# Performance work log

Measured on AMD Instinct MI355X. Metric: run time of the kernel, lower is better.

The kernel has to match this reference:

```python
import jax, jax.numpy as jnp
import numpy as np

B, Lq, C, NH, NP, DFF = 8, 10000, 256, 8, 4, 1024
H_IMG, W_IMG = 100, 100
HD = C // NH


def _layer_norm(x, g, b, eps=1e-5):
    m = jnp.mean(x, -1, keepdims=True)
    v = jnp.mean((x - m) ** 2, -1, keepdims=True)
    return (x - m) / jnp.sqrt(v + eps) * g + b


def _bilinear_sample(value, loc, Hs, Ws):
    # value: [B, Lin, NH, HD]; loc: [B, Lq, NH, NP, 2] normalized to [0,1]
    vt = jnp.transpose(value, (0, 2, 1, 3))  # [B, NH, Lin, HD]
    # move to [B, NH, Lq, NP] layout once; grid_sample(align_corners=False) pixel coords
    x = jnp.transpose(loc[..., 0], (0, 2, 1, 3)) * Ws - 0.5
    y = jnp.transpose(loc[..., 1], (0, 2, 1, 3)) * Hs - 0.5
    x0 = jnp.floor(x); y0 = jnp.floor(y)
    lx = x - x0; ly = y - y0

    def corner(xi, yi, w):
        valid = (xi >= 0) & (xi < Ws) & (yi >= 0) & (yi < Hs)
        xc = jnp.clip(xi, 0, Ws - 1).astype(jnp.int32)
        yc = jnp.clip(yi, 0, Hs - 1).astype(jnp.int32)
        idx = (yc * Ws + xc).reshape(B, NH, Lq * NP, 1)
        v = jnp.take_along_axis(vt, idx, axis=2).reshape(B, NH, Lq, NP, HD)
        return v * (w * valid)[..., None]

    acc = corner(x0, y0, (1 - lx) * (1 - ly))
    acc = acc + corner(x0 + 1, y0, lx * (1 - ly))
    acc = acc + corner(x0, y0 + 1, (1 - lx) * ly)
    acc = acc + corner(x0 + 1, y0 + 1, lx * ly)
    return acc  # [B, NH, Lq, NP, HD]


def setup_inputs() -> dict:
    key = jax.random.key(0)
    ks = jax.random.split(key, 12)
    s = 0.02
    return {
        "query": jax.random.normal(ks[0], (B, Lq, C), jnp.float32),
        "src": jax.random.normal(ks[1], (B, H_IMG * W_IMG, C), jnp.float32),
        "reference_points": jax.random.uniform(ks[2], (B, Lq, 1, 2), jnp.float32),
        "spatial_shapes": jnp.array([[H_IMG, W_IMG]], dtype=jnp.int64),
        "level_start_index": jnp.array([0], dtype=jnp.int64),
        "W_off": jax.random.normal(ks[3], (C, NH * NP * 2), jnp.float32) * s,
        "b_off": jnp.zeros((NH * NP * 2,), jnp.float32),
        "W_aw": jax.random.normal(ks[4], (C, NH * NP), jnp.float32) * s,
        "b_aw": jnp.zeros((NH * NP,), jnp.float32),
        "W_val": jax.random.normal(ks[5], (C, C), jnp.float32) * s,
        "b_val": jnp.zeros((C,), jnp.float32),
        "W_out": jax.random.normal(ks[6], (C, C), jnp.float32) * s,
        "b_out": jnp.zeros((C,), jnp.float32),
        "g1": jnp.ones((C,), jnp.float32),
        "be1": jnp.zeros((C,), jnp.float32),
        "W1": jax.random.normal(ks[7], (C, DFF), jnp.float32) * s,
        "b1": jnp.zeros((DFF,), jnp.float32),
        "W2": jax.random.normal(ks[8], (DFF, C), jnp.float32) * s,
        "b2": jnp.zeros((C,), jnp.float32),
        "g2": jnp.ones((C,), jnp.float32),
        "be2": jnp.zeros((C,), jnp.float32),
    }


def reference(query, src, reference_points, spatial_shapes, level_start_index,
              W_off, b_off, W_aw, b_aw, W_val, b_val, W_out, b_out,
              g1, be1, W1, b1, W2, b2, g2, be2):
    Hs = spatial_shapes[0, 0]
    Ws = spatial_shapes[0, 1]
    # MSDeformAttn (n_levels = 1)
    value = (src @ W_val + b_val).reshape(B, -1, NH, HD)
    off = (query @ W_off + b_off).reshape(B, Lq, NH, NP, 2)
    aw = jax.nn.softmax((query @ W_aw + b_aw).reshape(B, Lq, NH, NP), axis=-1)
    normalizer = jnp.stack([Ws, Hs]).astype(query.dtype)  # (W, H)
    loc = reference_points[:, :, None] + off / normalizer  # [B,Lq,NH,NP,2]
    sampled = _bilinear_sample(value, loc, Hs, Ws)  # [B,NH,Lq,NP,HD]
    attn = jnp.einsum('bhqpd,bqhp->bqhd', sampled, aw).reshape(B, Lq, C)
    attn = attn @ W_out + b_out
    # residual + LN + FFN + LN
    q = _layer_norm(query + attn, g1, be1)
    ffn = jax.nn.relu(q @ W1 + b1) @ W2 + b2
    return _layer_norm(q + ffn, g2, be2)
```

## Files before the change

kernel.cpp:

```cpp
#include <hip/hip_runtime.h>
#include <hip/hip_bf16.h>

typedef __hip_bfloat16 bf16;
typedef unsigned short u16;
typedef short short8 __attribute__((ext_vector_type(8)));
typedef float f32x4 __attribute__((ext_vector_type(4)));

static constexpr int B_   = 8;
static constexpr int Lq_  = 10000;
static constexpr int C_   = 256;
static constexpr int NH_  = 8;
static constexpr int NP_  = 4;
static constexpr int HIMG = 100;
static constexpr int WIMG = 100;
static constexpr int LIN  = 10000;

__device__ __forceinline__ u16 f2bf(float x) {
    union { bf16 b; u16 u; } cv; cv.b = __float2bfloat16(x); return cv.u;
}
__device__ __forceinline__ float bf2f(u16 u) {
    return __uint_as_float((unsigned)u << 16);
}

__device__ __forceinline__ void gl_lds16(const void* g, void* l) {
    __builtin_amdgcn_global_load_lds(
        (const __attribute__((address_space(1))) void*)g,
        (__attribute__((address_space(3))) void*)l, 16, 0, 0);
}
__device__ __forceinline__ void drain_barrier() {
    asm volatile("s_waitcnt vmcnt(0) lgkmcnt(0)" ::: "memory");
    __builtin_amdgcn_s_barrier();
}
#define LKW0() asm volatile("s_waitcnt lgkmcnt(0)" ::: "memory")
#define BAR()  __builtin_amdgcn_s_barrier()

template <bool AF32, bool LN>
__global__ __launch_bounds__(512, 2) void gemm256(
    const void* __restrict__ Av, const u16* __restrict__ Bg,
    const float* __restrict__ bias, const float* __restrict__ resid,
    const float* __restrict__ gw, const float* __restrict__ bw,
    u16* __restrict__ Co, int K)
{
    __shared__ __align__(16) u16 At[2][128 * 64];
    __shared__ __align__(16) u16 Bt[2][256 * 64];
    __shared__ float red[2][128][4];

    const int tid  = threadIdx.x;
    const int lane = tid & 63;
    const int w    = tid >> 6;
    const int wm   = w >> 2, wn = w & 3;
    const int m0   = blockIdx.x * 128;

    f32x4 acc[4][4];
#pragma unroll
    for (int i = 0; i < 4; ++i)
#pragma unroll
        for (int j = 0; j < 4; ++j) acc[i][j] = f32x4{0.f, 0.f, 0.f, 0.f};

    auto stageA = [&](int t) {
        const int kt = t << 6;
        if constexpr (AF32) {
            const int row = tid >> 2;
            const int k0  = (tid & 3) << 4;
            const float* s = (const float*)Av + (size_t)(m0 + row) * K + kt + k0;
            float4 v0 = *(const float4*)(s + 0);
            float4 v1 = *(const float4*)(s + 4);
            float4 v2 = *(const float4*)(s + 8);
            float4 v3 = *(const float4*)(s + 12);
            union { short8 s8; u16 u[8]; } ga, gb;
            ga.u[0]=f2bf(v0.x); ga.u[1]=f2bf(v0.y); ga.u[2]=f2bf(v0.z); ga.u[3]=f2bf(v0.w);
            ga.u[4]=f2bf(v1.x); ga.u[5]=f2bf(v1.y); ga.u[6]=f2bf(v1.z); ga.u[7]=f2bf(v1.w);
            gb.u[0]=f2bf(v2.x); gb.u[1]=f2bf(v2.y); gb.u[2]=f2bf(v2.z); gb.u[3]=f2bf(v2.w);
            gb.u[4]=f2bf(v3.x); gb.u[5]=f2bf(v3.y); gb.u[6]=f2bf(v3.z); gb.u[7]=f2bf(v3.w);
            u16* d = &At[t & 1][row * 64];
            *(short8*)&d[(k0)     ^ ((row & 7) << 3)] = ga.s8;
            *(short8*)&d[(k0 + 8) ^ ((row & 7) << 3)] = gb.s8;
        } else {
#pragma unroll
            for (int i = 0; i < 2; ++i) {
                const int rb  = w * 16 + i * 8;
                const int row = rb + (lane >> 3);
                const int gs  = (lane & 7) ^ (row & 7);
                gl_lds16((const u16*)Av + (size_t)(m0 + row) * K + kt + gs * 8,
                         &At[t & 1][rb * 64]);
            }
        }
    };
    auto stageB = [&](int t) {
        const int kt = t << 6;
#pragma unroll
        for (int i = 0; i < 4; ++i) {
            const int rb  = w * 32 + i * 8;
            const int row = rb + (lane >> 3);
            gl_lds16(Bg + (size_t)row * K + kt + (lane & 7) * 8,
                     &Bt[t & 1][rb * 64]);
        }
    };
    auto compute = [&](int t) {
        const u16* a = At[t & 1];
        const u16* b = Bt[t & 1];
#pragma unroll
        for (int ks = 0; ks < 2; ++ks) {
            const int ko = ks * 32 + ((lane >> 4) << 3);
            short8 bfr[4];
#pragma unroll
            for (int n = 0; n < 4; ++n) {
                const int nr = wn * 64 + n * 16 + (lane & 15);
                bfr[n] = *(const short8*)&b[nr * 64 + (ko ^ ((nr & 7) << 3))];
            }
#pragma unroll
            for (int m = 0; m < 4; ++m) {
                const int ar = wm * 64 + m * 16 + (lane & 15);
                const short8 af = *(const short8*)&a[ar * 64 + (ko ^ ((ar & 7) << 3))];
#pragma unroll
                for (int n = 0; n < 4; ++n)
                    acc[m][n] = __builtin_amdgcn_mfma_f32_16x16x32_bf16(
                        af, bfr[n], acc[m][n], 0, 0, 0);
            }
        }
    };

    stageA(0); stageB(0);
    drain_barrier();
    const int nt = K >> 6;
    for (int t = 0; t < nt; ++t) {
        if (t + 1 < nt) { stageA(t + 1); stageB(t + 1); }
        compute(t);
        drain_barrier();
    }

    float bcol[4], gcol[4], becol[4];
#pragma unroll
    for (int n = 0; n < 4; ++n) {
        const int col = wn * 64 + n * 16 + (lane & 15);
        bcol[n] = bias[col];
        if (LN) { gcol[n] = gw[col]; becol[n] = bw[col]; }
    }

    if constexpr (!LN) {
#pragma unroll
        for (int m = 0; m < 4; ++m)
#pragma unroll
            for (int r = 0; r < 4; ++r) {
                const int lr = wm * 64 + m * 16 + (lane >> 4) * 4 + r;
#pragma unroll
                for (int n = 0; n < 4; ++n) {
                    const int col = wn * 64 + n * 16 + (lane & 15);
                    Co[(size_t)(m0 + lr) * 256 + col] = f2bf(acc[m][n][r] + bcol[n]);
                }
            }
    } else {
        float s[4][4], s2[4][4];
#pragma unroll
        for (int m = 0; m < 4; ++m)
#pragma unroll
            for (int r = 0; r < 4; ++r) {
                const int lr = wm * 64 + m * 16 + (lane >> 4) * 4 + r;
                float ps = 0.f, ps2 = 0.f;
#pragma unroll
                for (int n = 0; n < 4; ++n) {
                    const int col = wn * 64 + n * 16 + (lane & 15);
                    float v = acc[m][n][r] + bcol[n]
                            + resid[(size_t)(m0 + lr) * 256 + col];
                    acc[m][n][r] = v;
                    ps += v; ps2 += v * v;
                }
#pragma unroll
                for (int o = 1; o < 16; o <<= 1) {
                    ps  += __shfl_xor(ps,  o);
                    ps2 += __shfl_xor(ps2, o);
                }
                s[m][r] = ps; s2[m][r] = ps2;
            }
        if ((lane & 15) == 0) {
#pragma unroll
            for (int m = 0; m < 4; ++m)
#pragma unroll
                for (int r = 0; r < 4; ++r) {
                    const int lr = wm * 64 + m * 16 + (lane >> 4) * 4 + r;
                    red[0][lr][wn] = s[m][r];
                    red[1][lr][wn] = s2[m][r];
                }
        }
        __syncthreads();
        if (tid < 128) {
            const float ss  = red[0][tid][0] + red[0][tid][1] + red[0][tid][2] + red[0][tid][3];
            const float ss2 = red[1][tid][0] + red[1][tid][1] + red[1][tid][2] + red[1][tid][3];
            const float mean = ss * (1.f / 256.f);
            const float var  = fmaxf(ss2 * (1.f / 256.f) - mean * mean, 0.f);
            red[0][tid][0] = mean;
            red[1][tid][0] = rsqrtf(var + 1e-5f);
        }
        __syncthreads();
#pragma unroll
        for (int m = 0; m < 4; ++m)
#pragma unroll
            for (int r = 0; r < 4; ++r) {
                const int lr = wm * 64 + m * 16 + (lane >> 4) * 4 + r;
                const float mean = red[0][lr][0];
                const float rstd = red[1][lr][0];
#pragma unroll
                for (int n = 0; n < 4; ++n) {
                    const int col = wn * 64 + n * 16 + (lane & 15);
                    const float o = (acc[m][n][r] - mean) * rstd * gcol[n] + becol[n];
                    Co[(size_t)(m0 + lr) * 256 + (col ^ ((lr & 7) << 3))] = f2bf(o);
                }
            }
    }
}

__global__ __launch_bounds__(512) void ffn_fused(
    const u16* __restrict__ q1b, const u16* __restrict__ W1f,
    const u16* __restrict__ W2f, const float* __restrict__ b1,
    const float* __restrict__ b2, const float* __restrict__ g2w,
    const float* __restrict__ be2, float* __restrict__ out)
{
    __shared__ __align__(16) u16 Asl[2][128 * 64];
    __shared__ __align__(16) u16 Hs[128 * 136];
    __shared__ __align__(16) u16 B1s[2][128 * 64];
    __shared__ __align__(16) u16 B2s[2][256 * 32];
    float (*red)[128][4] = (float (*)[128][4])Hs;

    const int tid  = threadIdx.x;
    const int lane = tid & 63;
    const int w    = tid >> 6;
    const int wm   = w >> 2, wn = w & 3;
    const int m0   = blockIdx.x * 128;
    const int ko   = (lane >> 4) << 3;

    int arow[4], aswz[4], hrow[4];
#pragma unroll
    for (int m = 0; m < 4; ++m) {
        const int ar = wm * 64 + m * 16 + (lane & 15);
        arow[m] = ar * 64; aswz[m] = (ar & 7) << 3; hrow[m] = ar * 136;
    }
    int b1r[2], b1x[2];
#pragma unroll
    for (int q = 0; q < 2; ++q) {
        const int nr = wn * 32 + q * 16 + (lane & 15);
        b1r[q] = nr * 64; b1x[q] = (nr & 7) << 3;
    }
    int b2i[4];
#pragma unroll
    for (int q = 0; q < 4; ++q) {
        const int nr = wn * 64 + q * 16 + (lane & 15);
        const int pr = nr >> 1;
        b2i[q] = pr * 64 + (nr & 1) * 32 + (ko ^ ((pr & 3) << 3));
    }

    f32x4 acc2[4][4];
#pragma unroll
    for (int i = 0; i < 4; ++i)
#pragma unroll
        for (int j = 0; j < 4; ++j) acc2[i][j] = f32x4{0.f, 0.f, 0.f, 0.f};

    auto stageAs = [&](int t, int buf) {
#pragma unroll
        for (int i = 0; i < 2; ++i) {
            const int rb = w * 16 + i * 8;
            gl_lds16(q1b + (size_t)(m0 + rb + (lane >> 3)) * 256 + t * 64 + (lane & 7) * 8,
                     &Asl[buf][rb * 64]);
        }
    };
    auto stageB1 = [&](int c, int t, int buf) {
#pragma unroll
        for (int i = 0; i < 2; ++i)
            gl_lds16(W1f + (size_t)(c * 4 + t) * 8192 + w * 1024 + i * 512 + lane * 8,
                     &B1s[buf][w * 1024 + i * 512]);
    };
    auto stageB2 = [&](int c, int u, int buf) {
#pragma unroll
        for (int i = 0; i < 2; ++i)
            gl_lds16(W2f + (size_t)(c * 4 + u) * 8192 + w * 1024 + i * 512 + lane * 8,
                     &B2s[buf][w * 1024 + i * 512]);
    };

    stageAs(0, 0); stageB1(0, 0, 0);
    drain_barrier();

    for (int c = 0; c < 8; ++c) {
        f32x4 acc1[4][2];
#pragma unroll
        for (int i = 0; i < 4; ++i)
#pragma unroll
            for (int j = 0; j < 2; ++j) acc1[i][j] = f32x4{0.f, 0.f, 0.f, 0.f};

        auto g1 = [&](int t) {
            const u16* a = Asl[t & 1];
            const u16* b = B1s[t & 1];
            __builtin_amdgcn_s_setprio(1);
#pragma unroll
            for (int ks = 0; ks < 2; ++ks) {
                const int kk = ks * 32 + ko;
                short8 bfr[2];
#pragma unroll
                for (int q = 0; q < 2; ++q)
                    bfr[q] = *(const short8*)&b[b1r[q] + (kk ^ b1x[q])];
#pragma unroll
                for (int m = 0; m < 4; ++m) {
                    const short8 af = *(const short8*)&a[arow[m] + (kk ^ aswz[m])];
#pragma unroll
                    for (int q = 0; q < 2; ++q)
                        acc1[m][q] = __builtin_amdgcn_mfma_f32_16x16x32_bf16(
                            af, bfr[q], acc1[m][q], 0, 0, 0);
                }
            }
            __builtin_amdgcn_s_setprio(0);
        };
        auto g2 = [&](int u) {
            const u16* b = B2s[u & 1];
            __builtin_amdgcn_s_setprio(1);
            short8 bfr[4];
#pragma unroll
            for (int q = 0; q < 4; ++q)
                bfr[q] = *(const short8*)&b[b2i[q]];
#pragma unroll
            for (int m = 0; m < 4; ++m) {
                const short8 af = *(const short8*)&Hs[hrow[m] + u * 32 + ko];
#pragma unroll
                for (int q = 0; q < 4; ++q)
                    acc2[m][q] = __builtin_amdgcn_mfma_f32_16x16x32_bf16(
                        af, bfr[q], acc2[m][q], 0, 0, 0);
            }
            __builtin_amdgcn_s_setprio(0);
        };

        stageAs(1, 1); stageB1(c, 1, 1);                   g1(0); drain_barrier();
        stageAs(2, 0); stageB1(c, 2, 0);                   g1(1); drain_barrier();
        stageAs(3, 1); stageB1(c, 3, 1); stageB2(c, 0, 0); g1(2); drain_barrier();
        stageB2(c, 1, 1);                                  g1(3); drain_barrier();

#pragma unroll
        for (int q = 0; q < 2; ++q) {
            const int col = wn * 32 + q * 16 + (lane & 15);
            const float bv = b1[c * 128 + col];
#pragma unroll
            for (int m = 0; m < 4; ++m)
#pragma unroll
                for (int r = 0; r < 4; ++r) {
                    const int row = wm * 64 + m * 16 + (lane >> 4) * 4 + r;
                    Hs[row * 136 + col] = f2bf(fmaxf(acc1[m][q][r] + bv, 0.f));
                }
        }
        LKW0(); BAR();

        g2(0); drain_barrier();
        stageB2(c, 2, 0);                                  g2(1); drain_barrier();
        if (c < 7) { stageAs(0, 0); stageB1(c + 1, 0, 0); }
        stageB2(c, 3, 1);                                  g2(2); drain_barrier();
        g2(3); drain_barrier();
    }

    float bcol[4], gcol[4], becol[4];
#pragma unroll
    for (int n = 0; n < 4; ++n) {
        const int col = wn * 64 + n * 16 + (lane & 15);
        bcol[n] = b2[col]; gcol[n] = g2w[col]; becol[n] = be2[col];
    }
    float s[4][4], s2[4][4];
#pragma unroll
    for (int m = 0; m < 4; ++m)
#pragma unroll
        for (int r = 0; r < 4; ++r) {
            const int lr = wm * 64 + m * 16 + (lane >> 4) * 4 + r;
            float ps = 0.f, ps2 = 0.f;
#pragma unroll
            for (int n = 0; n < 4; ++n) {
                const int col = wn * 64 + n * 16 + (lane & 15);
                const float q = bf2f(q1b[(size_t)(m0 + lr) * 256 + (col ^ ((lr & 7) << 3))]);
                const float v = acc2[m][n][r] + bcol[n] + q;
                acc2[m][n][r] = v;
                ps += v; ps2 += v * v;
            }
#pragma unroll
            for (int o = 1; o < 16; o <<= 1) {
                ps  += __shfl_xor(ps,  o);
                ps2 += __shfl_xor(ps2, o);
            }
            s[m][r] = ps; s2[m][r] = ps2;
        }
    if ((lane & 15) == 0) {
#pragma unroll
        for (int m = 0; m < 4; ++m)
#pragma unroll
            for (int r = 0; r < 4; ++r) {
                const int lr = wm * 64 + m * 16 + (lane >> 4) * 4 + r;
                red[0][lr][wn] = s[m][r];
                red[1][lr][wn] = s2[m][r];
            }
    }
    __syncthreads();
    if (tid < 128) {
        const float ss  = red[0][tid][0] + red[0][tid][1] + red[0][tid][2] + red[0][tid][3];
        const float ss2 = red[1][tid][0] + red[1][tid][1] + red[1][tid][2] + red[1][tid][3];
        const float mean = ss * (1.f / 256.f);
        const float var  = fmaxf(ss2 * (1.f / 256.f) - mean * mean, 0.f);
        red[0][tid][0] = mean;
        red[1][tid][0] = rsqrtf(var + 1e-5f);
    }
    __syncthreads();
#pragma unroll
    for (int m = 0; m < 4; ++m)
#pragma unroll
        for (int r = 0; r < 4; ++r) {
            const int lr = wm * 64 + m * 16 + (lane >> 4) * 4 + r;
            const float mean = red[0][lr][0];
            const float rstd = red[1][lr][0];
#pragma unroll
            for (int n = 0; n < 4; ++n) {
                const int col = wn * 64 + n * 16 + (lane & 15);
                out[(size_t)(m0 + lr) * 256 + col] =
                    (acc2[m][n][r] - mean) * rstd * gcol[n] + becol[n];
            }
        }
}

__global__ __launch_bounds__(256) void gemm_oaw(
    const float* __restrict__ Av, const u16* __restrict__ Bt,
    const float* __restrict__ bias, float* __restrict__ C,
    int M, int K, int Nreal, int ldc)
{
    __shared__ __align__(16) u16 Asl[2][128 * 32];
    __shared__ __align__(16) u16 Bsl[2][128 * 32];

    const int tid  = threadIdx.x;
    const int lane = tid & 63;
    const int w    = tid >> 6;
    const int wr   = (w >> 1) * 64;
    const int wc   = (w & 1) * 64;
    const int m0   = blockIdx.y * 128;
    const int n0   = blockIdx.x * 128;

    const int srow = lane >> 2;
    const int scol = (lane & 3) << 3;
    const u16* bG = Bt + (size_t)(n0 + w * 32 + srow) * K + scol;
    const size_t rstep16 = (size_t)16 * K;

    const int ar  = lane >> 3;
    const int ac  = (lane & 7) << 2;
    const float* aGf = Av + (size_t)(m0 + w * 32 + ar) * K + ac;

    const int aRoff = (wr + (lane & 15)) * 32 + (lane >> 4) * 8;
    const int bRoff = (wc + (lane & 15)) * 32 + (lane >> 4) * 8;

    f32x4 acc[4][4];
#pragma unroll
    for (int i = 0; i < 4; ++i)
#pragma unroll
        for (int j = 0; j < 4; ++j) acc[i][j] = f32x4{0.f, 0.f, 0.f, 0.f};

    float4 a4[4];
    const int nt = K >> 5;

#pragma unroll
    for (int rep = 0; rep < 4; ++rep)
        a4[rep] = *(const float4*)(aGf + (size_t)(rep * 8) * K);
#pragma unroll
    for (int rep = 0; rep < 4; ++rep) {
        ushort4 v{f2bf(a4[rep].x), f2bf(a4[rep].y), f2bf(a4[rep].z), f2bf(a4[rep].w)};
        *(ushort4*)&Asl[0][(w * 32 + rep * 8 + ar) * 32 + ac] = v;
    }
    gl_lds16(bG, &Bsl[0][(w * 32) * 32]);
    gl_lds16(bG + rstep16, &Bsl[0][(w * 32 + 16) * 32]);
    drain_barrier();

    for (int t = 0; t < nt; ++t) {
        const int cur = t & 1, nxt = cur ^ 1;
        const int k0n = (t + 1) << 5;
        const bool has_next = (t + 1 < nt);
        if (has_next) {
#pragma unroll
            for (int rep = 0; rep < 4; ++rep)
                a4[rep] = *(const float4*)(aGf + k0n + (size_t)(rep * 8) * K);
            gl_lds16(bG + k0n, &Bsl[nxt][(w * 32) * 32]);
            gl_lds16(bG + k0n + rstep16, &Bsl[nxt][(w * 32 + 16) * 32]);
        }
        short8 af[4], bfr[4];
#pragma unroll
        for (int m = 0; m < 4; ++m) af[m]  = *(const short8*)&Asl[cur][aRoff + m * 16 * 32];
#pragma unroll
        for (int n = 0; n < 4; ++n) bfr[n] = *(const short8*)&Bsl[cur][bRoff + n * 16 * 32];
#pragma unroll
        for (int m = 0; m < 4; ++m)
#pragma unroll
            for (int n = 0; n < 4; ++n)
                acc[m][n] = __builtin_amdgcn_mfma_f32_16x16x32_bf16(
                    af[m], bfr[n], acc[m][n], 0, 0, 0);
        if (has_next) {
#pragma unroll
            for (int rep = 0; rep < 4; ++rep) {
                ushort4 v{f2bf(a4[rep].x), f2bf(a4[rep].y), f2bf(a4[rep].z), f2bf(a4[rep].w)};
                *(ushort4*)&Asl[nxt][(w * 32 + rep * 8 + ar) * 32 + ac] = v;
            }
        }
        drain_barrier();
    }

#pragma unroll
    for (int n = 0; n < 4; ++n) {
        const int gc = n0 + wc + n * 16 + (lane & 15);
        if (gc >= Nreal) continue;
        const float bv = bias[gc];
        const int gr0 = m0 + wr + (lane >> 4) * 4;
#pragma unroll
        for (int m = 0; m < 4; ++m)
#pragma unroll
            for (int r = 0; r < 4; ++r)
                C[(size_t)(gr0 + m * 16 + r) * ldc + gc] = acc[m][n][r] + bv;
    }
}

__global__ __launch_bounds__(256) void prep_all(
    const float* __restrict__ Wv, const float* __restrict__ Wo,
    const float* __restrict__ W1, const float* __restrict__ W2,
    const float* __restrict__ Woff, const float* __restrict__ Waw,
    const float* __restrict__ boff, const float* __restrict__ baw,
    u16* __restrict__ Wvs, u16* __restrict__ Wos,
    u16* __restrict__ W1f, u16* __restrict__ W2f,
    u16* __restrict__ Woa, float* __restrict__ boa)
{
    const int idx = blockIdx.x * 256 + threadIdx.x;
    if (idx < 65536) {
        const int n = idx >> 8, kd = idx & 255;
        Wvs[idx] = f2bf(Wv[(size_t)(kd ^ ((n & 7) << 3)) * 256 + n]);
    } else if (idx < 131072) {
        const int i = idx - 65536, n = i >> 8, kd = i & 255;
        Wos[i] = f2bf(Wo[(size_t)(kd ^ ((n & 7) << 3)) * 256 + n]);
    } else if (idx < 393216) {
        const int i = idx - 131072;
        const int tile = i >> 13, si = i & 8191;
        const int c = tile >> 2, t = tile & 3;
        const int n = si >> 6, kd = si & 63;
        W1f[i] = f2bf(W1[(size_t)(t * 64 + (kd ^ ((n & 7) << 3))) * 1024 + c * 128 + n]);
    } else if (idx < 655360) {
        const int i = idx - 393216;
        const int tile = i >> 13, si = i & 8191;
        const int c = tile >> 2, u = tile & 3;
        const int pr = si >> 6, h = (si >> 5) & 1, e = si & 31;
        const int n = (pr << 1) | h;
        W2f[i] = f2bf(W2[(size_t)(c * 128 + u * 32 + (e ^ ((pr & 3) << 3))) * 256 + n]);
    } else if (idx < 688128) {
        const int i = idx - 655360, n = i >> 8, k = i & 255;
        float v = 0.f;
        if (n < 64)      v = Woff[(size_t)k * 64 + n];
        else if (n < 96) v = Waw[(size_t)k * 32 + (n - 64)];
        Woa[i] = f2bf(v);
    } else if (idx < 688256) {
        const int i = idx - 688128;
        boa[i] = (i < 64) ? boff[i] : (i < 96 ? baw[i - 64] : 0.f);
    }
}

__global__ __launch_bounds__(256) void sample_attn(
    const u16* __restrict__ val, const float* __restrict__ oaw,
    const float* __restrict__ refp, u16* __restrict__ attn)
{
    const int t   = threadIdx.x;
    const int gid = blockIdx.x * 64 + (t >> 2);
    const int c0  = (t & 3) << 3;
    const int h   = gid & (NH_ - 1);
    const int bq  = gid >> 3;

    const float* row = oaw + (size_t)bq * 96;
    const float rx = refp[(size_t)bq * 2 + 0] * (float)WIMG;
    const float ry = refp[(size_t)bq * 2 + 1] * (float)HIMG;

    const float4 aw4 = *(const float4*)(row + 64 + h * 4);
    const float mx = fmaxf(fmaxf(aw4.x, aw4.y), fmaxf(aw4.z, aw4.w));
    const float e0 = __expf(aw4.x - mx), e1 = __expf(aw4.y - mx);
    const float e2 = __expf(aw4.z - mx), e3 = __expf(aw4.w - mx);
    const float inv = 1.f / (e0 + e1 + e2 + e3);
    const float w4[4] = {e0 * inv, e1 * inv, e2 * inv, e3 * inv};

    const int b = bq / Lq_;
    const u16* vb = val + (size_t)b * LIN * C_ + h * 32 + c0;

    float acc[8] = {};
#pragma unroll
    for (int p = 0; p < NP_; ++p) {
        const float2 off = *(const float2*)(row + (h * 4 + p) * 2);
        const float x = rx + off.x - 0.5f;
        const float y = ry + off.y - 0.5f;
        const float xf = floorf(x), yf = floorf(y);
        const float lx = x - xf, ly = y - yf;
        const int x0 = (int)xf, y0 = (int)yf;
        const float wp = w4[p];
        const float w00 = wp * (1.f - lx) * (1.f - ly);
        const float w10 = wp * lx * (1.f - ly);
        const float w01 = wp * (1.f - lx) * ly;
        const float w11 = wp * lx * ly;

#pragma unroll
        for (int c = 0; c < 4; ++c) {
            const int xi = x0 + (c & 1);
            const int yi = y0 + (c >> 1);
            const float wc = (c == 0) ? w00 : (c == 1) ? w10 : (c == 2) ? w01 : w11;
            const bool v = ((unsigned)xi < (unsigned)WIMG) & ((unsigned)yi < (unsigned)HIMG);
            const int idx = v ? (yi * WIMG + xi) : 0;
            const float w = v ? wc : 0.f;
            const short8 d = *(const short8*)(vb + (size_t)idx * C_);
#pragma unroll
            for (int j = 0; j < 8; ++j)
                acc[j] = fmaf(w, bf2f(((const u16*)&d)[j]), acc[j]);
        }
    }

    union { short8 s; u16 u[8]; } o;
#pragma unroll
    for (int j = 0; j < 8; ++j) o.u[j] = f2bf(acc[j]);
    *(short8*)(attn + (size_t)bq * C_ + h * 32 + c0) = o.s;
}

extern "C" void kernel_launch(void* const* d_in, const int* in_sizes, int n_in,
                              void* d_out, int out_size, void* d_ws, size_t ws_size,
                              hipStream_t stream)
{
    const float* query = (const float*)d_in[0];
    const float* src   = (const float*)d_in[1];
    const float* refp  = (const float*)d_in[2];
    const float* W_off = (const float*)d_in[5];
    const float* b_off = (const float*)d_in[6];
    const float* W_aw  = (const float*)d_in[7];
    const float* b_aw  = (const float*)d_in[8];
    const float* W_val = (const float*)d_in[9];
    const float* b_val = (const float*)d_in[10];
    const float* W_out = (const float*)d_in[11];
    const float* b_out = (const float*)d_in[12];
    const float* g1    = (const float*)d_in[13];
    const float* be1   = (const float*)d_in[14];
    const float* W1    = (const float*)d_in[15];
    const float* b1    = (const float*)d_in[16];
    const float* W2    = (const float*)d_in[17];
    const float* b2    = (const float*)d_in[18];
    const float* g2    = (const float*)d_in[19];
    const float* be2   = (const float*)d_in[20];
    float* out = (float*)d_out;

    char* ws = (char*)d_ws;
    const int R = B_ * Lq_;

    u16*  val  = (u16*)(ws + 0);
    float* oaw = (float*)(ws + 40960000);
    u16*  attn = (u16*)(ws + 71680000);
    u16*  q1b  = (u16*)(ws + 112640000);
    u16*  Wvs  = (u16*)(ws + 153600000);
    u16*  Wos  = (u16*)(ws + 153600000 + 131072);
    u16*  W1f  = (u16*)(ws + 153600000 + 262144);
    u16*  W2f  = (u16*)(ws + 153600000 + 786432);
    u16*  Woa  = (u16*)(ws + 153600000 + 1310720);
    float* boa = (float*)(ws + 153600000 + 1376256);

    prep_all<<<2689, 256, 0, stream>>>(W_val, W_out, W1, W2, W_off, W_aw,
                                       b_off, b_aw, Wvs, Wos, W1f, W2f,
                                       Woa, boa);

    gemm256<true, false><<<625, 512, 0, stream>>>(
        src, Wvs, b_val, nullptr, nullptr, nullptr, val, 256);

    gemm_oaw<<<dim3(1, 625), 256, 0, stream>>>(
        query, Woa, boa, oaw, R, 256, 96, 96);

    sample_attn<<<10000, 256, 0, stream>>>(val, oaw, refp, attn);

    gemm256<false, true><<<625, 512, 0, stream>>>(
        attn, Wos, b_out, query, g1, be1, q1b, 256);

    ffn_fused<<<625, 512, 0, stream>>>(q1b, W1f, W2f, b1, b2, g2, be2, out);
}
```

Baseline: 333.7 us.

## Replace FFN double-buffering with a 12-slot LDS ring and pre-tiled operand layout

The fused FFN kernel now streams A, W1 and W2 tiles through a 12-entry LDS ring with partial vmcnt waits, so loads run several stages ahead instead of draining all memory traffic at every barrier. The LN epilogue of the out-projection GEMM writes q1 directly in a pre-tiled, swizzled 4096-element tile layout, and W1/W2 are repacked to match, so each ring slot is one contiguous 8 KB copy. The b1 bias is staged in LDS. This adds complex ring indexing and more LDS use, which may limit occupancy.

```diff
diff --git a/kernel.cpp b/kernel.cpp
--- a/kernel.cpp
+++ b/kernel.cpp
@@ -31,8 +31,10 @@
     asm volatile("s_waitcnt vmcnt(0) lgkmcnt(0)" ::: "memory");
     __builtin_amdgcn_s_barrier();
 }
+#define VMW(N) asm volatile("s_waitcnt vmcnt(" #N ")" ::: "memory")
 #define LKW0() asm volatile("s_waitcnt lgkmcnt(0)" ::: "memory")
 #define BAR()  __builtin_amdgcn_s_barrier()
+
 
 template <bool AF32, bool LN>
 __global__ __launch_bounds__(512, 2) void gemm256(
@@ -203,22 +205,23 @@
                 for (int n = 0; n < 4; ++n) {
                     const int col = wn * 64 + n * 16 + (lane & 15);
                     const float o = (acc[m][n][r] - mean) * rstd * gcol[n] + becol[n];
-                    Co[(size_t)(m0 + lr) * 256 + (col ^ ((lr & 7) << 3))] = f2bf(o);
+                    const int tt = col >> 5, ccol = col & 31, pr = lr >> 1;
+                    Co[((size_t)blockIdx.x * 8 + tt) * 4096
+                       + pr * 64 + (lr & 1) * 32 + (ccol ^ ((pr & 3) << 3))] = f2bf(o);
                 }
             }
     }
 }
 
-__global__ __launch_bounds__(512) void ffn_fused(
-    const u16* __restrict__ q1b, const u16* __restrict__ W1f,
-    const u16* __restrict__ W2f, const float* __restrict__ b1,
+__global__ __launch_bounds__(512) void ffn_deep(
+    const u16* __restrict__ q1p, const u16* __restrict__ W1p,
+    const u16* __restrict__ W2p, const float* __restrict__ b1,
     const float* __restrict__ b2, const float* __restrict__ g2w,
     const float* __restrict__ be2, float* __restrict__ out)
 {
-    __shared__ __align__(16) u16 Asl[2][128 * 64];
-    __shared__ __align__(16) u16 Hs[128 * 136];
-    __shared__ __align__(16) u16 B1s[2][128 * 64];
-    __shared__ __align__(16) u16 B2s[2][256 * 32];
+    __shared__ __align__(16) u16 ring[12][4096];
+    __shared__ __align__(16) u16 Hs[4][4096];
+    __shared__ __align__(16) float b1L[1024];
     float (*red)[128][4] = (float (*)[128][4])Hs;
 
     const int tid  = threadIdx.x;
@@ -228,24 +231,26 @@
     const int m0   = blockIdx.x * 128;
     const int ko   = (lane >> 4) << 3;
 
-    int arow[4], aswz[4], hrow[4];
+    int aoff[4];
 #pragma unroll
     for (int m = 0; m < 4; ++m) {
         const int ar = wm * 64 + m * 16 + (lane & 15);
-        arow[m] = ar * 64; aswz[m] = (ar & 7) << 3; hrow[m] = ar * 136;
-    }
-    int b1r[2], b1x[2];
+        const int pa = ar >> 1;
+        aoff[m] = pa * 64 + (ar & 1) * 32 + (ko ^ ((pa & 3) << 3));
+    }
+    int b1off[2];
 #pragma unroll
     for (int q = 0; q < 2; ++q) {
         const int nr = wn * 32 + q * 16 + (lane & 15);
-        b1r[q] = nr * 64; b1x[q] = (nr & 7) << 3;
-    }
-    int b2i[4];
-#pragma unroll
-    for (int q = 0; q < 4; ++q) {
-        const int nr = wn * 64 + q * 16 + (lane & 15);
         const int pr = nr >> 1;
-        b2i[q] = pr * 64 + (nr & 1) * 32 + (ko ^ ((pr & 3) << 3));
+        b1off[q] = pr * 64 + (nr & 1) * 32 + (ko ^ ((pr & 3) << 3));
+    }
+    int b2off[4];
+#pragma unroll
+    for (int nf = 0; nf < 4; ++nf) {
+        const int nr = (wn & 1) * 64 + nf * 16 + (lane & 15);
+        const int pr = nr >> 1;
+        b2off[nf] = pr * 64 + (nr & 1) * 32 + (ko ^ ((pr & 3) << 3));
     }
 
     f32x4 acc2[4][4];
@@ -254,102 +259,95 @@
 #pragma unroll
         for (int j = 0; j < 4; ++j) acc2[i][j] = f32x4{0.f, 0.f, 0.f, 0.f};
 
-    auto stageAs = [&](int t, int buf) {
-#pragma unroll
-        for (int i = 0; i < 2; ++i) {
-            const int rb = w * 16 + i * 8;
-            gl_lds16(q1b + (size_t)(m0 + rb + (lane >> 3)) * 256 + t * 64 + (lane & 7) * 8,
-                     &Asl[buf][rb * 64]);
-        }
+    auto issue = [&](int g) {
+        if (g >= 192) g -= 192;
+        const int cc = g / 24;
+        const int r  = g - cc * 24;
+        const u16* src;
+        if (r < 16) {
+            const int t = r >> 1;
+            src = (r & 1) ? W1p + ((size_t)(cc * 8 + t)) * 4096
+                          : q1p + ((size_t)(blockIdx.x * 8 + t)) * 4096;
+        } else {
+            src = W2p + ((size_t)(cc * 8 + (r - 16))) * 4096;
+        }
+        gl_lds16(src + w * 512 + lane * 8, &ring[g % 12][w * 512]);
     };
-    auto stageB1 = [&](int c, int t, int buf) {
-#pragma unroll
-        for (int i = 0; i < 2; ++i)
-            gl_lds16(W1f + (size_t)(c * 4 + t) * 8192 + w * 1024 + i * 512 + lane * 8,
-                     &B1s[buf][w * 1024 + i * 512]);
-    };
-    auto stageB2 = [&](int c, int u, int buf) {
-#pragma unroll
-        for (int i = 0; i < 2; ++i)
-            gl_lds16(W2f + (size_t)(c * 4 + u) * 8192 + w * 1024 + i * 512 + lane * 8,
-                     &B2s[buf][w * 1024 + i * 512]);
-    };
-
-    stageAs(0, 0); stageB1(0, 0, 0);
-    drain_barrier();
-
-    for (int c = 0; c < 8; ++c) {
+
+    gl_lds16(b1 + (w & 3) * 256 + lane * 4, &b1L[(w & 3) * 256]);
+    for (int g = 0; g < 10; ++g) issue(g);
+    VMW(8); BAR();
+
+    int gbase = 0;
+    for (int c = 0; c < 8; ++c, gbase += 24) {
         f32x4 acc1[4][2];
 #pragma unroll
         for (int i = 0; i < 4; ++i)
 #pragma unroll
             for (int j = 0; j < 2; ++j) acc1[i][j] = f32x4{0.f, 0.f, 0.f, 0.f};
 
-        auto g1 = [&](int t) {
-            const u16* a = Asl[t & 1];
-            const u16* b = B1s[t & 1];
+#pragma unroll
+        for (int t = 0; t < 8; ++t) {
+            issue(gbase + 2 * t + 10);
+            issue(gbase + 2 * t + 11);
+            const u16* aT = ring[(2 * t) % 12];
+            const u16* bT = ring[(2 * t + 1) % 12];
+            const short8 bf0 = *(const short8*)&bT[b1off[0]];
+            const short8 bf1 = *(const short8*)&bT[b1off[1]];
             __builtin_amdgcn_s_setprio(1);
 #pragma unroll
-            for (int ks = 0; ks < 2; ++ks) {
-                const int kk = ks * 32 + ko;
-                short8 bfr[2];
-#pragma unroll
-                for (int q = 0; q < 2; ++q)
-                    bfr[q] = *(const short8*)&b[b1r[q] + (kk ^ b1x[q])];
-#pragma unroll
-                for (int m = 0; m < 4; ++m) {
-                    const short8 af = *(const short8*)&a[arow[m] + (kk ^ aswz[m])];
-#pragma unroll
-                    for (int q = 0; q < 2; ++q)
-                        acc1[m][q] = __builtin_amdgcn_mfma_f32_16x16x32_bf16(
-                            af, bfr[q], acc1[m][q], 0, 0, 0);
-                }
+            for (int m = 0; m < 4; ++m) {
+                const short8 af = *(const short8*)&aT[aoff[m]];
+                acc1[m][0] = __builtin_amdgcn_mfma_f32_16x16x32_bf16(
+                    af, bf0, acc1[m][0], 0, 0, 0);
+                acc1[m][1] = __builtin_amdgcn_mfma_f32_16x16x32_bf16(
+                    af, bf1, acc1[m][1], 0, 0, 0);
             }
             __builtin_amdgcn_s_setprio(0);
-        };
-        auto g2 = [&](int u) {
-            const u16* b = B2s[u & 1];
-            __builtin_amdgcn_s_setprio(1);
-            short8 bfr[4];
-#pragma unroll
-            for (int q = 0; q < 4; ++q)
-                bfr[q] = *(const short8*)&b[b2i[q]];
-#pragma unroll
-            for (int m = 0; m < 4; ++m) {
-                const short8 af = *(const short8*)&Hs[hrow[m] + u * 32 + ko];
-#pragma unroll
-                for (int q = 0; q < 4; ++q)
-                    acc2[m][q] = __builtin_amdgcn_mfma_f32_16x16x32_bf16(
-                        af, bfr[q], acc2[m][q], 0, 0, 0);
-            }
-            __builtin_amdgcn_s_setprio(0);
-        };
-
-        stageAs(1, 1); stageB1(c, 1, 1);                   g1(0); drain_barrier();
-        stageAs(2, 0); stageB1(c, 2, 0);                   g1(1); drain_barrier();
-        stageAs(3, 1); stageB1(c, 3, 1); stageB2(c, 0, 0); g1(2); drain_barrier();
-        stageB2(c, 1, 1);                                  g1(3); drain_barrier();
+            VMW(8); BAR();
+        }
 
 #pragma unroll
         for (int q = 0; q < 2; ++q) {
             const int col = wn * 32 + q * 16 + (lane & 15);
-            const float bv = b1[c * 128 + col];
+            const float bv = b1L[c * 128 + col];
+            const int ut = col >> 5, ccol = col & 31;
 #pragma unroll
             for (int m = 0; m < 4; ++m)
 #pragma unroll
                 for (int r = 0; r < 4; ++r) {
                     const int row = wm * 64 + m * 16 + (lane >> 4) * 4 + r;
-                    Hs[row * 136 + col] = f2bf(fmaxf(acc1[m][q][r] + bv, 0.f));
+                    const int pr = row >> 1;
+                    Hs[ut][pr * 64 + (row & 1) * 32 + (ccol ^ ((pr & 3) << 3))] =
+                        f2bf(fmaxf(acc1[m][q][r] + bv, 0.f));
                 }
         }
         LKW0(); BAR();
 
-        g2(0); drain_barrier();
-        stageB2(c, 2, 0);                                  g2(1); drain_barrier();
-        if (c < 7) { stageAs(0, 0); stageB1(c + 1, 0, 0); }
-        stageB2(c, 3, 1);                                  g2(2); drain_barrier();
-        g2(3); drain_barrier();
-    }
+#pragma unroll
+        for (int u = 0; u < 4; ++u) {
+            issue(gbase + 26 + 2 * u);
+            issue(gbase + 27 + 2 * u);
+            const u16* bT = ring[(16 + 2 * u + (wn >> 1)) % 12];
+            short8 bfr[4];
+#pragma unroll
+            for (int nf = 0; nf < 4; ++nf)
+                bfr[nf] = *(const short8*)&bT[b2off[nf]];
+            __builtin_amdgcn_s_setprio(1);
+#pragma unroll
+            for (int m = 0; m < 4; ++m) {
+                const short8 af = *(const short8*)&Hs[u][aoff[m]];
+#pragma unroll
+                for (int nf = 0; nf < 4; ++nf)
+                    acc2[m][nf] = __builtin_amdgcn_mfma_f32_16x16x32_bf16(
+                        af, bfr[nf], acc2[m][nf], 0, 0, 0);
+            }
+            __builtin_amdgcn_s_setprio(0);
+            VMW(8); BAR();
+        }
+    }
+    asm volatile("s_waitcnt vmcnt(0)" ::: "memory");
+    BAR();
 
     float bcol[4], gcol[4], becol[4];
 #pragma unroll
@@ -363,11 +361,14 @@
 #pragma unroll
         for (int r = 0; r < 4; ++r) {
             const int lr = wm * 64 + m * 16 + (lane >> 4) * 4 + r;
+            const int pr = lr >> 1;
             float ps = 0.f, ps2 = 0.f;
 #pragma unroll
             for (int n = 0; n < 4; ++n) {
                 const int col = wn * 64 + n * 16 + (lane & 15);
-                const float q = bf2f(q1b[(size_t)(m0 + lr) * 256 + (col ^ ((lr & 7) << 3))]);
+                const int tt = col >> 5, ccol = col & 31;
+                const float q = bf2f(q1p[((size_t)blockIdx.x * 8 + tt) * 4096
+                    + pr * 64 + (lr & 1) * 32 + (ccol ^ ((pr & 3) << 3))]);
                 const float v = acc2[m][n][r] + bcol[n] + q;
                 acc2[m][n][r] = v;
                 ps += v; ps2 += v * v;
@@ -516,7 +517,7 @@
     const float* __restrict__ Woff, const float* __restrict__ Waw,
     const float* __restrict__ boff, const float* __restrict__ baw,
     u16* __restrict__ Wvs, u16* __restrict__ Wos,
-    u16* __restrict__ W1f, u16* __restrict__ W2f,
+    u16* __restrict__ W1p, u16* __restrict__ W2p,
     u16* __restrict__ Woa, float* __restrict__ boa)
 {
     const int idx = blockIdx.x * 256 + threadIdx.x;
@@ -528,17 +529,21 @@
         Wos[i] = f2bf(Wo[(size_t)(kd ^ ((n & 7) << 3)) * 256 + n]);
     } else if (idx < 393216) {
         const int i = idx - 131072;
-        const int tile = i >> 13, si = i & 8191;
-        const int c = tile >> 2, t = tile & 3;
-        const int n = si >> 6, kd = si & 63;
-        W1f[i] = f2bf(W1[(size_t)(t * 64 + (kd ^ ((n & 7) << 3))) * 1024 + c * 128 + n]);
+        const int tile = i >> 12, si = i & 4095;
+        const int c = tile >> 3, t = tile & 7;
+        const int pr = si >> 6, h = (si >> 5) & 1, e = si & 31;
+        const int nr = (pr << 1) | h;
+        const int kk = e ^ ((pr & 3) << 3);
+        W1p[i] = f2bf(W1[(size_t)(t * 32 + kk) * 1024 + c * 128 + nr]);
     } else if (idx < 655360) {
         const int i = idx - 393216;
-        const int tile = i >> 13, si = i & 8191;
-        const int c = tile >> 2, u = tile & 3;
+        const int tile = i >> 12, si = i & 4095;
+        const int c = tile >> 3, j = tile & 7;
+        const int u = j >> 1, half = j & 1;
         const int pr = si >> 6, h = (si >> 5) & 1, e = si & 31;
-        const int n = (pr << 1) | h;
-        W2f[i] = f2bf(W2[(size_t)(c * 128 + u * 32 + (e ^ ((pr & 3) << 3))) * 256 + n]);
+        const int nr = (pr << 1) | h;
+        const int kk = e ^ ((pr & 3) << 3);
+        W2p[i] = f2bf(W2[(size_t)(c * 128 + u * 32 + kk) * 256 + half * 128 + nr]);
     } else if (idx < 688128) {
         const int i = idx - 655360, n = i >> 8, k = i & 255;
         float v = 0.f;
@@ -642,16 +647,16 @@
     u16*  val  = (u16*)(ws + 0);
     float* oaw = (float*)(ws + 40960000);
     u16*  attn = (u16*)(ws + 71680000);
-    u16*  q1b  = (u16*)(ws + 112640000);
+    u16*  q1p  = (u16*)(ws + 112640000);
     u16*  Wvs  = (u16*)(ws + 153600000);
     u16*  Wos  = (u16*)(ws + 153600000 + 131072);
-    u16*  W1f  = (u16*)(ws + 153600000 + 262144);
-    u16*  W2f  = (u16*)(ws + 153600000 + 786432);
+    u16*  W1p  = (u16*)(ws + 153600000 + 262144);
+    u16*  W2p  = (u16*)(ws + 153600000 + 786432);
     u16*  Woa  = (u16*)(ws + 153600000 + 1310720);
     float* boa = (float*)(ws + 153600000 + 1376256);
 
     prep_all<<<2689, 256, 0, stream>>>(W_val, W_out, W1, W2, W_off, W_aw,
-                                       b_off, b_aw, Wvs, Wos, W1f, W2f,
+                                       b_off, b_aw, Wvs, Wos, W1p, W2p,
                                        Woa, boa);
 
     gemm256<true, false><<<625, 512, 0, stream>>>(
@@ -663,7 +668,7 @@
     sample_attn<<<10000, 256, 0, stream>>>(val, oaw, refp, attn);
 
     gemm256<false, true><<<625, 512, 0, stream>>>(
-        attn, Wos, b_out, query, g1, be1, q1b, 256);
-
-    ffn_fused<<<625, 512, 0, stream>>>(q1b, W1f, W2f, b1, b2, g2, be2, out);
-}
+        attn, Wos, b_out, query, g1, be1, q1p, 256);
+
+    ffn_deep<<<625, 512, 0, stream>>>(q1p, W1p, W2p, b1, b2, g2, be2, out);
+}
```

Result: no change. 327.5 us (-1.9%).
